# Kernel optimization log

Measured on AMD Instinct MI355X. Metric: run time of the kernel, lower is better.

The kernel has to match this reference:

```python
import jax, jax.numpy as jnp
import numpy as np

B, N, C = 2, 2048, 1024
H, HD = 16, 64
PX, PY, PS = 24, 24, 16  # S2RoPE head_dim split (px+py+ps == head_dim)


def rotate_half(t):
    t1, t2 = jnp.split(t, 2, axis=-1)
    return jnp.concatenate([-t2, t1], axis=-1)


def apply_phase_rope(t, phase):
    # t: [B, N, H, d_seg] (d_seg even), phase: [B, N, d_seg//2] angles in radians
    ang = jnp.concatenate([phase, phase], axis=-1)[:, :, None, :]  # [B,N,1,d_seg]
    return t * jnp.cos(ang) + rotate_half(t) * jnp.sin(ang)


def s2rope(t, phase_x, phase_y, phase_sph):
    # spherical RoPE: rotate three disjoint segments of head_dim by the
    # per-token x / y / spherical phases
    tx, ty, ts = t[..., :PX], t[..., PX:PX + PY], t[..., PX + PY:]
    return jnp.concatenate([
        apply_phase_rope(tx, phase_x),
        apply_phase_rope(ty, phase_y),
        apply_phase_rope(ts, phase_sph),
    ], axis=-1)


def setup_inputs() -> dict:
    key = jax.random.key(0)
    ks = jax.random.split(key, 9)
    two_pi = 6.2831853
    return {
        "x": jax.random.normal(ks[0], (B, N, C), dtype=jnp.float32),
        "phase_x": jax.random.uniform(ks[1], (B, N, PX // 2), dtype=jnp.float32) * two_pi,
        "phase_y": jax.random.uniform(ks[2], (B, N, PY // 2), dtype=jnp.float32) * two_pi,
        "phase_sph": jax.random.uniform(ks[3], (B, N, PS // 2), dtype=jnp.float32) * two_pi,
        "rope_mask": jax.random.randint(ks[4], (B, N), 0, 2).astype(bool),
        "Wqkv": jax.random.normal(ks[5], (C, 3 * C), dtype=jnp.float32) * (C ** -0.5),
        "bqkv": jax.random.normal(ks[6], (3 * C,), dtype=jnp.float32) * 0.02,
        "Wproj": jax.random.normal(ks[7], (C, C), dtype=jnp.float32) * (C ** -0.5),
        "bproj": jax.random.normal(ks[8], (C,), dtype=jnp.float32) * 0.02,
    }


def reference(x, phase_x, phase_y, phase_sph, rope_mask, Wqkv, bqkv, Wproj, bproj):
    # qkv projection -> [B, N, 3, H, HD]
    qkv = (x @ Wqkv + bqkv).reshape(B, N, 3, H, HD)
    q, k, v = qkv[:, :, 0], qkv[:, :, 1], qkv[:, :, 2]  # each [B, N, H, HD]

    # template path: S2RoPE with rope_mask selecting which tokens are rotated
    q_rope = s2rope(q, phase_x, phase_y, phase_sph)
    k_rope = s2rope(k, phase_x, phase_y, phase_sph)
    m = rope_mask[:, :, None, None]  # [B, N, 1, 1]
    q = jnp.where(m, q_rope, q)
    k = jnp.where(m, k_rope, k)

    scale = HD ** -0.5
    # [B, H, N, N] scores, softmax over keys, then weighted sum of values
    attn = jax.nn.softmax(jnp.einsum('bnhd,bmhd->bhnm', q, k) * scale, axis=-1)
    out = jnp.einsum('bhnm,bmhd->bnhd', attn, v).reshape(B, N, C)
    return out @ Wproj + bproj
```

## Files before the change

### kernel.cpp

```cpp
#include <hip/hip_runtime.h>
#include <hip/hip_fp16.h>

typedef _Float16 f16;
typedef unsigned int u32;
typedef _Float16 f16x4 __attribute__((ext_vector_type(4)));
typedef _Float16 f16x8 __attribute__((ext_vector_type(8)));
typedef float f32x4 __attribute__((ext_vector_type(4)));
typedef float f32x16 __attribute__((ext_vector_type(16)));

#define B_  2
#define N_  2048
#define C_  1024
#define H_  16
#define HD_ 64

__device__ __forceinline__ void gload_lds16(const void* g, void* l) {
  __builtin_amdgcn_global_load_lds((const __attribute__((address_space(1))) u32*)g,
                                   (__attribute__((address_space(3))) u32*)l,
                                   16, 0, 0);
}

__device__ __forceinline__ u32 pack_f16(float a, float b) {
  auto h2 = __builtin_amdgcn_cvt_pkrtz(a, b);
  return __builtin_bit_cast(u32, h2);
}

__device__ __forceinline__ float max3f(float a, float b, float c) {
  return fmaxf(fmaxf(a, b), c);
}

__global__ void detect_mask(const u32* __restrict__ m, int* __restrict__ flag) {
  __shared__ int bad;
  if (threadIdx.x == 0) bad = 0;
  __syncthreads();
  int v = 0;
  for (int i = threadIdx.x; i < 1024; i += 256) {
    u32 w = m[i];
    if (w != 0u && w != 1u && w != 0x3F800000u) v = 1;
  }
  if (v) atomicOr(&bad, 1);
  __syncthreads();
  if (threadIdx.x == 0) *flag = bad;
}

__global__ __launch_bounds__(256) void phase_tab(const float* __restrict__ px,
                                                 const float* __restrict__ py,
                                                 const float* __restrict__ psp,
                                                 const void* __restrict__ maskPtr,
                                                 const int* __restrict__ maskFlag,
                                                 float* __restrict__ cs_tab,
                                                 float* __restrict__ sn_tab) {
  const int idx = blockIdx.x * 256 + threadIdx.x;
  const int j = idx & 31, tn = idx >> 5;
  const int byteMode = *maskFlag;
  const bool doRope = byteMode ? (((const unsigned char*)maskPtr)[tn] != 0)
                               : (((const u32*)maskPtr)[tn] != 0u);
  float c = 1.f, s = 0.f;
  if (doRope) {
    float ph;
    if (j < 12)      ph = px[tn * 12 + j];
    else if (j < 24) ph = py[tn * 12 + (j - 12)];
    else             ph = psp[tn * 8 + (j - 24)];
    c = __cosf(ph);
    s = __sinf(ph);
  }
  cs_tab[idx] = c;
  sn_tab[idx] = s;
}

__global__ __launch_bounds__(256) void cvt_x(const float* __restrict__ in,
                                             f16* __restrict__ out, int n8) {
  const int i = blockIdx.x * 256 + threadIdx.x;
  if (i >= n8) return;
  const float4 a = ((const float4*)in)[i * 2];
  const float4 b = ((const float4*)in)[i * 2 + 1];
  f16x8 o = {(f16)a.x, (f16)a.y, (f16)a.z, (f16)a.w,
             (f16)b.x, (f16)b.y, (f16)b.z, (f16)b.w};
  ((f16x8*)out)[i] = o;
}

__global__ __launch_bounds__(256) void transpose_cvt(const float* __restrict__ W,
                                                     f16* __restrict__ Wt,
                                                     int R, int Ccols) {
  __shared__ __align__(16) f16 tile[32][34];
  const int c0 = blockIdx.x * 32, r0 = blockIdx.y * 32;
  const int tx = threadIdx.x, ty = threadIdx.y;
#pragma unroll
  for (int k = 0; k < 4; ++k)
    tile[ty + 8 * k][tx] = (f16)W[(size_t)(r0 + ty + 8 * k) * Ccols + c0 + tx];
  __syncthreads();
#pragma unroll
  for (int k = 0; k < 4; ++k)
    Wt[(size_t)(c0 + ty + 8 * k) * R + r0 + tx] = tile[tx][ty + 8 * k];
}

template <bool OUT_F32>
__global__ __launch_bounds__(256) void gemm_bt(const f16* __restrict__ A,
                                               const f16* __restrict__ Bt,
                                               const float* __restrict__ bias,
                                               void* __restrict__ Cout,
                                               int M, int N, int K) {
  __shared__ __align__(16) f16 As[128 * 64];
  __shared__ __align__(16) f16 Bs[128 * 64];
  const int tid = threadIdx.x;
  const int lane = tid & 63;
  const int wv = tid >> 6;
  const int wm = wv >> 1, wn = wv & 1;
  const int nTN = N >> 7;
  int bid = blockIdx.x;
  const int cpx = gridDim.x >> 3;
  bid = (bid & 7) * cpx + (bid >> 3);
  const int tM = bid / nTN, tN = bid % nTN;
  const int rowBase = tM << 7, colBase = tN << 7;
  const int cl = lane & 15, cg = lane >> 4;

  f32x4 acc[4][4];
#pragma unroll
  for (int i = 0; i < 4; ++i)
#pragma unroll
    for (int j = 0; j < 4; ++j) acc[i][j] = (f32x4){0.f, 0.f, 0.f, 0.f};

  const int sR = tid >> 3, sC = tid & 7;

  for (int k0 = 0; k0 < K; k0 += 64) {
#pragma unroll
    for (int is = 0; is < 4; ++is) {
      const int r = is * 32 + sR;
      const int sc = sC ^ (r & 7);
      gload_lds16(A + (size_t)(rowBase + r) * K + k0 + sc * 8, As + is * 2048 + tid * 8);
    }
#pragma unroll
    for (int is = 0; is < 4; ++is) {
      const int r = is * 32 + sR;
      const int sc = sC ^ (r & 7);
      gload_lds16(Bt + (size_t)(colBase + r) * K + k0 + sc * 8, Bs + is * 2048 + tid * 8);
    }
    asm volatile("s_waitcnt vmcnt(0)" ::: "memory");
    __syncthreads();

#pragma unroll
    for (int ks = 0; ks < 2; ++ks) {
      f16x8 af[4], bf[4];
#pragma unroll
      for (int m = 0; m < 4; ++m) {
        const int row = wm * 64 + m * 16 + cl;
        const int ck = (ks * 4 + cg) ^ (row & 7);
        af[m] = *(const f16x8*)(As + row * 64 + ck * 8);
      }
#pragma unroll
      for (int n = 0; n < 4; ++n) {
        const int row = wn * 64 + n * 16 + cl;
        const int ck = (ks * 4 + cg) ^ (row & 7);
        bf[n] = *(const f16x8*)(Bs + row * 64 + ck * 8);
      }
#pragma unroll
      for (int m = 0; m < 4; ++m)
#pragma unroll
        for (int n = 0; n < 4; ++n)
          acc[m][n] = __builtin_amdgcn_mfma_f32_16x16x32_f16(af[m], bf[n], acc[m][n], 0, 0, 0);
    }
    __syncthreads();
  }

#pragma unroll
  for (int m = 0; m < 4; ++m) {
#pragma unroll
    for (int n = 0; n < 4; ++n) {
      const int gr0 = rowBase + wm * 64 + m * 16 + cg * 4;
      const int gc = colBase + wn * 64 + n * 16 + cl;
      const float bz = bias[gc];
#pragma unroll
      for (int reg = 0; reg < 4; ++reg) {
        const float v = acc[m][n][reg] + bz;
        if (OUT_F32)
          ((float*)Cout)[(size_t)(gr0 + reg) * N + gc] = v;
        else
          ((f16*)Cout)[(size_t)(gr0 + reg) * N + gc] = (f16)v;
      }
    }
  }
}

__global__ __launch_bounds__(256) void rope_split(const f16* __restrict__ qkv,
                                                  const float* __restrict__ cs_tab,
                                                  const float* __restrict__ sn_tab,
                                                  f16* __restrict__ Qh,
                                                  f16* __restrict__ Kh,
                                                  f16* __restrict__ Vt) {
  __shared__ float cs[64][32], sn[64][32];
  __shared__ __align__(16) f16 vtile[64][72];
  const int tid = threadIdx.x;
  const int blk = blockIdx.x;
  const int hg = blk & 3;
  const int nt = (blk >> 2) & 31;
  const int b = blk >> 7;
  const int n0 = nt * 64;

  for (int i = tid; i < 64 * 32; i += 256) {
    const int tk = i >> 5, j = i & 31;
    const size_t gi = ((size_t)b * N_ + n0 + tk) * 32 + j;
    cs[tk][j] = cs_tab[gi];
    sn[tk][j] = sn_tab[gi];
  }
  __syncthreads();

  const int tk = tid >> 2, hl = tid & 3;
  const int h = hg * 4 + hl;
  const int n = n0 + tk;
  const size_t inRow = ((size_t)b * N_ + n) * 3072 + (size_t)h * 64;
  const size_t outRow = (((size_t)(b * H_ + h)) * N_ + n) * 64;

#pragma unroll
  for (int sec = 0; sec < 2; ++sec) {
    const f16* src = qkv + inRow + sec * 1024;
    float t[64];
#pragma unroll
    for (int c = 0; c < 8; ++c) {
      f16x8 v = *(const f16x8*)(src + c * 8);
#pragma unroll
      for (int j = 0; j < 8; ++j) t[c * 8 + j] = (float)v[j];
    }
    __align__(16) f16 o[64];
#pragma unroll
    for (int d = 0; d < 64; ++d) {
      int j;
      float rot;
      if (d < 24) {
        j = (d < 12) ? d : d - 12;
        rot = (d < 12) ? -t[d + 12] : t[d - 12];
      } else if (d < 48) {
        const int dd = d - 24;
        j = 12 + ((dd < 12) ? dd : dd - 12);
        rot = (dd < 12) ? -t[d + 12] : t[d - 12];
      } else {
        const int dd = d - 48;
        j = 24 + ((dd < 8) ? dd : dd - 8);
        rot = (dd < 8) ? -t[d + 8] : t[d - 8];
      }
      o[d] = (f16)(t[d] * cs[tk][j] + rot * sn[tk][j]);
    }
    f16* dst = (sec == 0 ? Qh : Kh) + outRow;
#pragma unroll
    for (int c = 0; c < 8; ++c) *(f16x8*)(dst + c * 8) = *(const f16x8*)(o + c * 8);
  }

  for (int hl2 = 0; hl2 < 4; ++hl2) {
    const int h2 = hg * 4 + hl2;
    __syncthreads();
    {
      const int tk2 = tid >> 2, c2 = tid & 3;
      const size_t srow = ((size_t)b * N_ + n0 + tk2) * 3072 + 2048 + (size_t)h2 * 64 + c2 * 16;
      *(f16x8*)(&vtile[tk2][c2 * 16]) = *(const f16x8*)(qkv + srow);
      *(f16x8*)(&vtile[tk2][c2 * 16 + 8]) = *(const f16x8*)(qkv + srow + 8);
    }
    __syncthreads();
    {
      const int d = tid >> 2, seg = tid & 3;
      __align__(16) f16 tmp[16];
#pragma unroll
      for (int i = 0; i < 16; ++i) tmp[i] = vtile[seg * 16 + i][d];
      const size_t drow = (((size_t)(b * H_ + h2)) * 64 + d) * N_ + n0 + seg * 16;
      *(f16x8*)(Vt + drow) = *(const f16x8*)(tmp);
      *(f16x8*)(Vt + drow + 8) = *(const f16x8*)(tmp + 8);
    }
  }
}

__global__ __launch_bounds__(256) void attn2(const f16* __restrict__ Qh,
                                             const f16* __restrict__ Kh,
                                             const f16* __restrict__ Vt,
                                             f16* __restrict__ Y) {
  __shared__ __align__(16) f16 lds_flat[3 * 8192];
  const int tid = threadIdx.x, lane = tid & 63, w = tid >> 6;
  int bid = blockIdx.x;
  bid = (bid & 7) * 64 + (bid >> 3);
  const int bh = bid >> 4, qb = bid & 15;
  const int b = bh >> 4, h = bh & 15;
  const f16* Qb = Qh + (size_t)bh * N_ * 64;
  const f16* Kb = Kh + (size_t)bh * N_ * 64;
  const f16* Vb = Vt + (size_t)bh * 64 * N_;
  const int ql = lane & 31, hi = lane >> 5;

  f16x8 qf[4];
  {
    const int qrow = qb * 128 + w * 32 + ql;
    const f16 scl = (f16)0.125f;
#pragma unroll
    for (int ks = 0; ks < 4; ++ks) {
      f16x8 v = *(const f16x8*)(Qb + (size_t)qrow * 64 + ks * 16 + hi * 8);
#pragma unroll
      for (int j = 0; j < 8; ++j) v[j] *= scl;
      qf[ks] = v;
    }
  }

  f32x16 Of[2];
#pragma unroll
  for (int d = 0; d < 2; ++d)
#pragma unroll
    for (int r = 0; r < 16; ++r) Of[d][r] = 0.f;
  float m_run = -1e30f, l_run = 0.f;

  const int sr = tid >> 3, sc = tid & 7;
#define STAGE(t, bp)                                                                     \
  {                                                                                      \
    _Pragma("unroll") for (int i = 0; i < 2; ++i) {                                      \
      const int row = i * 32 + sr;                                                       \
      const int g = sc ^ (row & 7);                                                      \
      gload_lds16(Kb + (size_t)((t) * 64 + row) * 64 + g * 8, (bp) + i * 2048 + tid * 8);\
    }                                                                                    \
    _Pragma("unroll") for (int i = 0; i < 2; ++i) {                                      \
      const int row = i * 32 + sr;                                                       \
      const int g = sc ^ (row & 7);                                                      \
      gload_lds16(Vb + (size_t)row * N_ + (t) * 64 + g * 8,                              \
                  (bp) + 4096 + i * 2048 + tid * 8);                                     \
    }                                                                                    \
  }

#define SOFTMAX_CHUNK(sa)                                                                \
  {                                                                                      \
    float t0 = max3f(sa[0], sa[1], sa[2]);                                               \
    float t1 = max3f(sa[3], sa[4], sa[5]);                                               \
    float t2 = max3f(sa[6], sa[7], sa[8]);                                               \
    float t3 = max3f(sa[9], sa[10], sa[11]);                                             \
    float t4 = max3f(sa[12], sa[13], sa[14]);                                            \
    float pmax = max3f(max3f(t0, t1, t2), max3f(t3, t4, sa[15]), -1e30f);                \
    pmax = fmaxf(pmax, __shfl_xor(pmax, 32));                                            \
    if (__any(pmax > m_run + 8.0f)) {                                                    \
      const float mnew = fmaxf(m_run, pmax);                                             \
      const float corr = __expf(m_run - mnew);                                           \
      l_run *= corr;                                                                     \
      _Pragma("unroll") for (int d = 0; d < 2; ++d)                                      \
        _Pragma("unroll") for (int r = 0; r < 16; ++r) Of[d][r] *= corr;                 \
      m_run = mnew;                                                                      \
    }                                                                                    \
    _Pragma("unroll") for (int r = 0; r < 16; ++r) sa[r] = __expf(sa[r] - m_run);        \
    float s0 = ((sa[0] + sa[1]) + (sa[2] + sa[3])) + ((sa[4] + sa[5]) + (sa[6] + sa[7]));\
    float s1 = ((sa[8] + sa[9]) + (sa[10] + sa[11])) +                                   \
               ((sa[12] + sa[13]) + (sa[14] + sa[15]));                                  \
    l_run += s0 + s1;                                                                    \
  }

#define PV_CHUNK(sa, s)                                                                  \
  {                                                                                      \
    u32 pw[8];                                                                           \
    _Pragma("unroll") for (int tt = 0; tt < 8; ++tt)                                     \
      pw[tt] = pack_f16(sa[2 * tt], sa[2 * tt + 1]);                                     \
    _Pragma("unroll") for (int kk = 0; kk < 2; ++kk) {                                   \
      u32 a0 = pw[4 * kk], a1 = pw[4 * kk + 1];                                          \
      u32 b0 = pw[4 * kk + 2], b1 = pw[4 * kk + 3];                                      \
      asm volatile("v_permlane32_swap_b32 %0, %1" : "+v"(a0), "+v"(b0));                 \
      asm volatile("v_permlane32_swap_b32 %0, %1" : "+v"(a1), "+v"(b1));                 \
      union { u32 u[4]; f16x8 v; } pf;                                                   \
      pf.u[0] = a0; pf.u[1] = a1; pf.u[2] = b0; pf.u[3] = b1;                            \
      __builtin_amdgcn_s_setprio(1);                                                     \
      _Pragma("unroll") for (int df = 0; df < 2; ++df) {                                 \
        const int d = df * 32 + ql;                                                      \
        f16x8 vf = *(const f16x8*)(Vs + d * 64 + (((s) * 4 + kk * 2 + hi) ^ (d & 7)) * 8);\
        Of[df] = __builtin_amdgcn_mfma_f32_32x32x16_f16(vf, pf.v, Of[df], 0, 0, 0);      \
      }                                                                                  \
      __builtin_amdgcn_s_setprio(0);                                                     \
    }                                                                                    \
  }

  f16* const base = &lds_flat[0];
  STAGE(0, base);
  STAGE(1, base + 8192);
  asm volatile("s_waitcnt vmcnt(4)" ::: "memory");
  __builtin_amdgcn_s_barrier();

  f16* curp = base;
  f16* stagep = base + 16384;
  for (int t = 0; t < N_ / 64; ++t) {
    if (t < N_ / 64 - 2) STAGE(t + 2, stagep);
    const f16* Ks = curp;
    const f16* Vs = curp + 4096;

    f32x16 sa0, sa1;
#pragma unroll
    for (int r = 0; r < 16; ++r) { sa0[r] = 0.f; sa1[r] = 0.f; }
    const int krow0 = ql, krow1 = 32 + ql;
    __builtin_amdgcn_s_setprio(1);
#pragma unroll
    for (int ks = 0; ks < 4; ++ks) {
      f16x8 kf = *(const f16x8*)(Ks + krow0 * 64 + ((ks * 2 + hi) ^ (krow0 & 7)) * 8);
      sa0 = __builtin_amdgcn_mfma_f32_32x32x16_f16(kf, qf[ks], sa0, 0, 0, 0);
    }
#pragma unroll
    for (int ks = 0; ks < 4; ++ks) {
      f16x8 kf = *(const f16x8*)(Ks + krow1 * 64 + ((ks * 2 + hi) ^ (krow1 & 7)) * 8);
      sa1 = __builtin_amdgcn_mfma_f32_32x32x16_f16(kf, qf[ks], sa1, 0, 0, 0);
    }
    __builtin_amdgcn_s_setprio(0);

    SOFTMAX_CHUNK(sa0);
    PV_CHUNK(sa0, 0);
    SOFTMAX_CHUNK(sa1);
    PV_CHUNK(sa1, 1);

    if (t < N_ / 64 - 2)
      asm volatile("s_waitcnt vmcnt(4) lgkmcnt(0)" ::: "memory");
    else if (t < N_ / 64 - 1)
      asm volatile("s_waitcnt vmcnt(0) lgkmcnt(0)" ::: "memory");
    else
      asm volatile("s_waitcnt lgkmcnt(0)" ::: "memory");
    __builtin_amdgcn_s_barrier();
    curp = (curp == base + 16384) ? base : curp + 8192;
    stagep = (stagep == base + 16384) ? base : stagep + 8192;
  }

  const float l_tot = l_run + __shfl_xor(l_run, 32);
  const float inv = 1.0f / l_tot;
  f16* Ow = base + w * (32 * 72);
#pragma unroll
  for (int df = 0; df < 2; ++df)
#pragma unroll
    for (int g = 0; g < 4; ++g) {
      f16x4 ov;
#pragma unroll
      for (int e = 0; e < 4; ++e) ov[e] = (f16)(Of[df][g * 4 + e] * inv);
      *(f16x4*)(Ow + ql * 72 + df * 32 + g * 8 + hi * 4) = ov;
    }
  __syncthreads();
  const int rr = lane >> 1, half = lane & 1;
  const f16* srcp = Ow + rr * 72 + half * 32;
  const int nglob = qb * 128 + w * 32 + rr;
  f16* dst = Y + ((size_t)b * N_ + nglob) * C_ + h * 64 + half * 32;
#pragma unroll
  for (int c2 = 0; c2 < 4; ++c2)
    *(f16x8*)(dst + c2 * 8) = *(const f16x8*)(srcp + c2 * 8);
}

extern "C" void kernel_launch(void* const* d_in, const int* in_sizes, int n_in,
                              void* d_out, int out_size, void* d_ws, size_t ws_size,
                              hipStream_t stream) {
  const float* x = (const float*)d_in[0];
  const float* px = (const float*)d_in[1];
  const float* py = (const float*)d_in[2];
  const float* psp = (const float*)d_in[3];
  const void* mask = (const void*)d_in[4];
  const float* Wqkv = (const float*)d_in[5];
  const float* bqkv = (const float*)d_in[6];
  const float* Wproj = (const float*)d_in[7];
  const float* bproj = (const float*)d_in[8];
  float* out = (float*)d_out;
  char* ws = (char*)d_ws;

  f16* xh     = (f16*)(ws + 0);
  f16* Wqkvt  = (f16*)(ws + 8388608);
  f16* Wprojt = (f16*)(ws + 14680064);
  f16* qkvh   = (f16*)(ws + 16777216);
  f16* Qh     = (f16*)(ws + 41943040);
  f16* Kh     = (f16*)(ws + 50331648);
  f16* Vt     = (f16*)(ws + 58720256);
  f16* Yh     = (f16*)(ws + 67108864);
  int* mflag  = (int*)(ws + 75497472);
  float* cs_tab = (float*)(ws + 67108864);
  float* sn_tab = (float*)(ws + 67108864 + 524288);

  detect_mask<<<1, 256, 0, stream>>>((const u32*)mask, mflag);
  cvt_x<<<2048, 256, 0, stream>>>(x, xh, (B_ * N_ * C_) / 8);
  phase_tab<<<512, 256, 0, stream>>>(px, py, psp, mask, mflag, cs_tab, sn_tab);
  transpose_cvt<<<dim3(96, 32), dim3(32, 8), 0, stream>>>(Wqkv, Wqkvt, C_, 3 * C_);
  transpose_cvt<<<dim3(32, 32), dim3(32, 8), 0, stream>>>(Wproj, Wprojt, C_, C_);
  gemm_bt<false><<<(4096 / 128) * (3072 / 128), 256, 0, stream>>>(
      xh, Wqkvt, bqkv, (void*)qkvh, 4096, 3072, 1024);
  rope_split<<<256, 256, 0, stream>>>(qkvh, cs_tab, sn_tab, Qh, Kh, Vt);
  attn2<<<512, 256, 0, stream>>>(Qh, Kh, Vt, Yh);
  gemm_bt<true><<<(4096 / 128) * (1024 / 128), 256, 0, stream>>>(
      Yh, Wprojt, bproj, (void*)out, 4096, 1024, 1024);
}
```

Measured before the change: 160.2 us.

## Fuse RoPE and Q/K/V head-split into the QKV GEMM epilogue

The QKV projection GEMM now stages its 128x128 output tile in shared memory and applies the S2RoPE rotation and head-major Q/K layout (or the V transpose) directly in the epilogue. This removes the separate rope_split kernel and the write and re-read of the full fp16 qkv intermediate. In exchange the epilogue gains an extra LDS pass and reads cos/sin tables from global memory per thread. The V-transpose reads in the epilogue may hit LDS bank conflicts.

```diff
diff --git a/kernel.cpp b/kernel.cpp
--- a/kernel.cpp
+++ b/kernel.cpp
@@ -94,19 +94,23 @@
     Wt[(size_t)(c0 + ty + 8 * k) * R + r0 + tx] = tile[tx][ty + 8 * k];
 }
 
-template <bool OUT_F32>
-__global__ __launch_bounds__(256) void gemm_bt(const f16* __restrict__ A,
-                                               const f16* __restrict__ Bt,
-                                               const float* __restrict__ bias,
-                                               void* __restrict__ Cout,
-                                               int M, int N, int K) {
-  __shared__ __align__(16) f16 As[128 * 64];
-  __shared__ __align__(16) f16 Bs[128 * 64];
+__global__ __launch_bounds__(256) void gemm_qkv(const f16* __restrict__ A,
+                                                const f16* __restrict__ Bt,
+                                                const float* __restrict__ bias,
+                                                const float* __restrict__ cs_tab,
+                                                const float* __restrict__ sn_tab,
+                                                f16* __restrict__ Qh,
+                                                f16* __restrict__ Kh,
+                                                f16* __restrict__ Vt) {
+  __shared__ __align__(16) f16 smem[128 * 130];
+  f16* const As = smem;
+  f16* const Bs = smem + 8192;
+  const int K = 1024, Ncols = 3072;
   const int tid = threadIdx.x;
   const int lane = tid & 63;
   const int wv = tid >> 6;
   const int wm = wv >> 1, wn = wv & 1;
-  const int nTN = N >> 7;
+  const int nTN = Ncols >> 7;
   int bid = blockIdx.x;
   const int cpx = gridDim.x >> 3;
   bid = (bid & 7) * cpx + (bid >> 3);
@@ -163,63 +167,38 @@
   }
 
 #pragma unroll
-  for (int m = 0; m < 4; ++m) {
+  for (int m = 0; m < 4; ++m)
 #pragma unroll
     for (int n = 0; n < 4; ++n) {
-      const int gr0 = rowBase + wm * 64 + m * 16 + cg * 4;
-      const int gc = colBase + wn * 64 + n * 16 + cl;
-      const float bz = bias[gc];
+      const int lc = wn * 64 + n * 16 + cl;
+      const float bz = bias[colBase + lc];
 #pragma unroll
       for (int reg = 0; reg < 4; ++reg) {
-        const float v = acc[m][n][reg] + bz;
-        if (OUT_F32)
-          ((float*)Cout)[(size_t)(gr0 + reg) * N + gc] = v;
-        else
-          ((f16*)Cout)[(size_t)(gr0 + reg) * N + gc] = (f16)v;
+        const int lr = wm * 64 + m * 16 + cg * 4 + reg;
+        smem[lr * 130 + lc] = (f16)(acc[m][n][reg] + bz);
       }
     }
-  }
-}
-
-__global__ __launch_bounds__(256) void rope_split(const f16* __restrict__ qkv,
-                                                  const float* __restrict__ cs_tab,
-                                                  const float* __restrict__ sn_tab,
-                                                  f16* __restrict__ Qh,
-                                                  f16* __restrict__ Kh,
-                                                  f16* __restrict__ Vt) {
-  __shared__ float cs[64][32], sn[64][32];
-  __shared__ __align__(16) f16 vtile[64][72];
-  const int tid = threadIdx.x;
-  const int blk = blockIdx.x;
-  const int hg = blk & 3;
-  const int nt = (blk >> 2) & 31;
-  const int b = blk >> 7;
-  const int n0 = nt * 64;
-
-  for (int i = tid; i < 64 * 32; i += 256) {
-    const int tk = i >> 5, j = i & 31;
-    const size_t gi = ((size_t)b * N_ + n0 + tk) * 32 + j;
-    cs[tk][j] = cs_tab[gi];
-    sn[tk][j] = sn_tab[gi];
-  }
   __syncthreads();
 
-  const int tk = tid >> 2, hl = tid & 3;
-  const int h = hg * 4 + hl;
-  const int n = n0 + tk;
-  const size_t inRow = ((size_t)b * N_ + n) * 3072 + (size_t)h * 64;
-  const size_t outRow = (((size_t)(b * H_ + h)) * N_ + n) * 64;
-
-#pragma unroll
-  for (int sec = 0; sec < 2; ++sec) {
-    const f16* src = qkv + inRow + sec * 1024;
+  const int sec = colBase >> 10;
+  const int h0 = (colBase & 1023) >> 6;
+  const int bb = rowBase >> 11;
+  const int nbase = rowBase & 2047;
+
+  if (sec < 2) {
+    const int lr = tid >> 1, hh = tid & 1;
+    const int n = nbase + lr;
+    const int h = h0 + hh;
+    const f16* srcrow = smem + lr * 130 + hh * 64;
     float t[64];
 #pragma unroll
     for (int c = 0; c < 8; ++c) {
-      f16x8 v = *(const f16x8*)(src + c * 8);
+      f16x8 v = *(const f16x8*)(srcrow + c * 8);
 #pragma unroll
       for (int j = 0; j < 8; ++j) t[c * 8 + j] = (float)v[j];
     }
+    const float* csr = cs_tab + ((size_t)bb * N_ + n) * 32;
+    const float* snr = sn_tab + ((size_t)bb * N_ + n) * 32;
     __align__(16) f16 o[64];
 #pragma unroll
     for (int d = 0; d < 64; ++d) {
@@ -237,31 +216,101 @@
         j = 24 + ((dd < 8) ? dd : dd - 8);
         rot = (dd < 8) ? -t[d + 8] : t[d - 8];
       }
-      o[d] = (f16)(t[d] * cs[tk][j] + rot * sn[tk][j]);
-    }
-    f16* dst = (sec == 0 ? Qh : Kh) + outRow;
+      o[d] = (f16)(t[d] * csr[j] + rot * snr[j]);
+    }
+    f16* dst = (sec == 0 ? Qh : Kh) + (((size_t)(bb * H_ + h)) * N_ + n) * 64;
 #pragma unroll
     for (int c = 0; c < 8; ++c) *(f16x8*)(dst + c * 8) = *(const f16x8*)(o + c * 8);
-  }
-
-  for (int hl2 = 0; hl2 < 4; ++hl2) {
-    const int h2 = hg * 4 + hl2;
+  } else {
+    const int pr = tid >> 1, half = tid & 1;
+    const int hh = pr >> 6, d = pr & 63;
+    const int h = h0 + hh;
+    __align__(16) f16 o[64];
+#pragma unroll
+    for (int i = 0; i < 64; ++i) o[i] = smem[(half * 64 + i) * 130 + hh * 64 + d];
+    f16* dst = Vt + (((size_t)(bb * H_ + h)) * 64 + d) * N_ + nbase + half * 64;
+#pragma unroll
+    for (int c = 0; c < 8; ++c) *(f16x8*)(dst + c * 8) = *(const f16x8*)(o + c * 8);
+  }
+}
+
+__global__ __launch_bounds__(256) void gemm_bt_f32(const f16* __restrict__ A,
+                                                   const f16* __restrict__ Bt,
+                                                   const float* __restrict__ bias,
+                                                   float* __restrict__ Cout,
+                                                   int M, int N, int K) {
+  __shared__ __align__(16) f16 As[128 * 64];
+  __shared__ __align__(16) f16 Bs[128 * 64];
+  const int tid = threadIdx.x;
+  const int lane = tid & 63;
+  const int wv = tid >> 6;
+  const int wm = wv >> 1, wn = wv & 1;
+  const int nTN = N >> 7;
+  int bid = blockIdx.x;
+  const int cpx = gridDim.x >> 3;
+  bid = (bid & 7) * cpx + (bid >> 3);
+  const int tM = bid / nTN, tN = bid % nTN;
+  const int rowBase = tM << 7, colBase = tN << 7;
+  const int cl = lane & 15, cg = lane >> 4;
+
+  f32x4 acc[4][4];
+#pragma unroll
+  for (int i = 0; i < 4; ++i)
+#pragma unroll
+    for (int j = 0; j < 4; ++j) acc[i][j] = (f32x4){0.f, 0.f, 0.f, 0.f};
+
+  const int sR = tid >> 3, sC = tid & 7;
+
+  for (int k0 = 0; k0 < K; k0 += 64) {
+#pragma unroll
+    for (int is = 0; is < 4; ++is) {
+      const int r = is * 32 + sR;
+      const int sc = sC ^ (r & 7);
+      gload_lds16(A + (size_t)(rowBase + r) * K + k0 + sc * 8, As + is * 2048 + tid * 8);
+    }
+#pragma unroll
+    for (int is = 0; is < 4; ++is) {
+      const int r = is * 32 + sR;
+      const int sc = sC ^ (r & 7);
+      gload_lds16(Bt + (size_t)(colBase + r) * K + k0 + sc * 8, Bs + is * 2048 + tid * 8);
+    }
+    asm volatile("s_waitcnt vmcnt(0)" ::: "memory");
     __syncthreads();
-    {
-      const int tk2 = tid >> 2, c2 = tid & 3;
-      const size_t srow = ((size_t)b * N_ + n0 + tk2) * 3072 + 2048 + (size_t)h2 * 64 + c2 * 16;
-      *(f16x8*)(&vtile[tk2][c2 * 16]) = *(const f16x8*)(qkv + srow);
-      *(f16x8*)(&vtile[tk2][c2 * 16 + 8]) = *(const f16x8*)(qkv + srow + 8);
+
+#pragma unroll
+    for (int ks = 0; ks < 2; ++ks) {
+      f16x8 af[4], bf[4];
+#pragma unroll
+      for (int m = 0; m < 4; ++m) {
+        const int row = wm * 64 + m * 16 + cl;
+        const int ck = (ks * 4 + cg) ^ (row & 7);
+        af[m] = *(const f16x8*)(As + row * 64 + ck * 8);
+      }
+#pragma unroll
+      for (int n = 0; n < 4; ++n) {
+        const int row = wn * 64 + n * 16 + cl;
+        const int ck = (ks * 4 + cg) ^ (row & 7);
+        bf[n] = *(const f16x8*)(Bs + row * 64 + ck * 8);
+      }
+#pragma unroll
+      for (int m = 0; m < 4; ++m)
+#pragma unroll
+        for (int n = 0; n < 4; ++n)
+          acc[m][n] = __builtin_amdgcn_mfma_f32_16x16x32_f16(af[m], bf[n], acc[m][n], 0, 0, 0);
     }
     __syncthreads();
-    {
-      const int d = tid >> 2, seg = tid & 3;
-      __align__(16) f16 tmp[16];
-#pragma unroll
-      for (int i = 0; i < 16; ++i) tmp[i] = vtile[seg * 16 + i][d];
-      const size_t drow = (((size_t)(b * H_ + h2)) * 64 + d) * N_ + n0 + seg * 16;
-      *(f16x8*)(Vt + drow) = *(const f16x8*)(tmp);
-      *(f16x8*)(Vt + drow + 8) = *(const f16x8*)(tmp + 8);
+  }
+
+#pragma unroll
+  for (int m = 0; m < 4; ++m) {
+#pragma unroll
+    for (int n = 0; n < 4; ++n) {
+      const int gr0 = rowBase + wm * 64 + m * 16 + cg * 4;
+      const int gc = colBase + wn * 64 + n * 16 + cl;
+      const float bz = bias[gc];
+#pragma unroll
+      for (int reg = 0; reg < 4; ++reg)
+        Cout[(size_t)(gr0 + reg) * N + gc] = acc[m][n][reg] + bz;
     }
   }
 }
@@ -449,24 +498,22 @@
   f16* xh     = (f16*)(ws + 0);
   f16* Wqkvt  = (f16*)(ws + 8388608);
   f16* Wprojt = (f16*)(ws + 14680064);
-  f16* qkvh   = (f16*)(ws + 16777216);
   f16* Qh     = (f16*)(ws + 41943040);
   f16* Kh     = (f16*)(ws + 50331648);
   f16* Vt     = (f16*)(ws + 58720256);
   f16* Yh     = (f16*)(ws + 67108864);
   int* mflag  = (int*)(ws + 75497472);
-  float* cs_tab = (float*)(ws + 67108864);
-  float* sn_tab = (float*)(ws + 67108864 + 524288);
+  float* cs_tab = (float*)(ws + 16777216);
+  float* sn_tab = (float*)(ws + 16777216 + 524288);
 
   detect_mask<<<1, 256, 0, stream>>>((const u32*)mask, mflag);
   cvt_x<<<2048, 256, 0, stream>>>(x, xh, (B_ * N_ * C_) / 8);
   phase_tab<<<512, 256, 0, stream>>>(px, py, psp, mask, mflag, cs_tab, sn_tab);
   transpose_cvt<<<dim3(96, 32), dim3(32, 8), 0, stream>>>(Wqkv, Wqkvt, C_, 3 * C_);
   transpose_cvt<<<dim3(32, 32), dim3(32, 8), 0, stream>>>(Wproj, Wprojt, C_, C_);
-  gemm_bt<false><<<(4096 / 128) * (3072 / 128), 256, 0, stream>>>(
-      xh, Wqkvt, bqkv, (void*)qkvh, 4096, 3072, 1024);
-  rope_split<<<256, 256, 0, stream>>>(qkvh, cs_tab, sn_tab, Qh, Kh, Vt);
+  gemm_qkv<<<(4096 / 128) * (3072 / 128), 256, 0, stream>>>(
+      xh, Wqkvt, bqkv, cs_tab, sn_tab, Qh, Kh, Vt);
   attn2<<<512, 256, 0, stream>>>(Qh, Kh, Vt, Yh);
-  gemm_bt<true><<<(4096 / 128) * (1024 / 128), 256, 0, stream>>>(
-      Yh, Wprojt, bproj, (void*)out, 4096, 1024, 1024);
-}
+  gemm_bt_f32<<<(4096 / 128) * (1024 / 128), 256, 0, stream>>>(
+      Yh, Wprojt, bproj, out, 4096, 1024, 1024);
+}
```

Result: faster. 153.1 us (-4.5%).
